# Kernel optimization log

Hardware: AMD Instinct MI355X
Metric: run time of the kernel (lower is better)

## Reference

```python
import jax, jax.numpy as jnp
import numpy as np

ALPHA = 0.1          # LeakyReLU negative slope
NEG = -9.0e15        # mask fill value (matches torch source)
S_OUT = 64           # source_out_features
T_OUT = 64           # target_out_features


def setup_inputs() -> dict:
    key = jax.random.key(0)
    ks = jax.random.split(key, 8)
    n_s, n_t = 8192, 4096
    s_in, t_in = 128, 128
    hs = jax.random.normal(ks[0], (n_s, s_in), dtype=jnp.float32)
    ht = jax.random.normal(ks[1], (n_t, t_in), dtype=jnp.float32)
    A_opt = jax.random.randint(ks[2], (n_t, n_s), 0, 2, dtype=jnp.int32)
    # xavier_uniform with gain=1.414
    def xavier(k, shape, gain=1.414):
        fan_in, fan_out = shape[0], shape[1]
        bound = gain * np.sqrt(6.0 / (fan_in + fan_out))
        return jax.random.uniform(k, shape, jnp.float32, -bound, bound)
    Ws = xavier(ks[3], (s_in, T_OUT))
    Wt = xavier(ks[4], (t_in, S_OUT))
    a1 = xavier(ks[5], (S_OUT + T_OUT, 1))
    bias_s = jnp.zeros((T_OUT,), jnp.float32)
    bias_t = jnp.zeros((S_OUT,), jnp.float32)
    return {"hs": hs, "ht": ht, "A_opt": A_opt, "Ws": Ws, "Wt": Wt,
            "a1": a1, "bias_s": bias_s, "bias_t": bias_t}


def reference(hs, ht, A_opt, Ws, Wt, a1, bias_s, bias_t):
    # Asymmetric HOAN, eval mode (dropout=0), concatenate=True.
    Whs = hs @ Ws                       # [n_s, t_out]
    Wht = ht @ Wt                       # [n_t, s_out]
    # a1 split: first S_OUT rows pair with Wht, remaining T_OUT rows with Whs
    a_t = a1[:S_OUT, :]                 # [s_out, 1]
    a_s = a1[S_OUT:, :]                 # [t_out, 1]
    Whst = Whs @ a_s                    # [n_s, 1]
    Whtt = Wht @ a_t                    # [n_t, 1]
    e_st = jax.nn.leaky_relu(Whtt + Whst.T, ALPHA)   # [n_t, n_s]
    e_ts = jax.nn.leaky_relu(Whst + Whtt.T, ALPHA)   # [n_s, n_t]
    mask = A_opt > 0                    # [n_t, n_s]
    att_st = jax.nn.softmax(jnp.where(mask, e_st, NEG), axis=1)
    h_prime_st = att_st @ Whs + bias_s  # [n_t, t_out]
    att_ts = jax.nn.softmax(jnp.where(mask.T, e_ts, NEG), axis=1)
    h_prime_ts = att_ts @ Wht + bias_t  # [n_s, s_out]
    return jax.nn.elu(h_prime_st), jax.nn.elu(h_prime_ts)
```

## Files before the change

### kernel.cpp

```cpp
#include <hip/hip_runtime.h>
#include <math.h>

#define N_S 8192
#define N_T 4096
#define DIN 128
#define NF  64
#define SPL0 8
#define SPL1 4

typedef __attribute__((ext_vector_type(8))) short short8;
typedef __attribute__((ext_vector_type(4))) float f32x4;
typedef __attribute__((ext_vector_type(4))) int i32x4;
typedef unsigned long long u64;
typedef unsigned int u32;

__device__ __forceinline__ unsigned short f2bf(float x){
  unsigned u = __float_as_uint(x);
  unsigned r = (u + 0x7fffu + ((u >> 16) & 1u)) >> 16;
  return (unsigned short)r;
}

__device__ __forceinline__ size_t xt2_idx(int f, int k){
  return ((size_t)(k >> 5))*2048 + (size_t)((f >> 4)*512 + ((k >> 3) & 3)*128 + (f & 15)*8 + (k & 7));
}

__global__ __launch_bounds__(256) void k1_fused(
    const int* __restrict__ A,
    u64* __restrict__ RBt,
    const float* __restrict__ hs, const float* __restrict__ ht,
    const float* __restrict__ Ws, const float* __restrict__ Wt,
    const float* __restrict__ a1,
    unsigned short* __restrict__ XT2s, unsigned short* __restrict__ XT2t,
    float* __restrict__ EFs, float* __restrict__ EFt)
{
  __shared__ __align__(16) float smem[DIN*NF + 4*DIN];
  int bx = blockIdx.x;
  int t = threadIdx.x;
  if (bx < 2048) {
    u64* rbS = (u64*)smem;
    int w = t >> 6, l = t & 63;
    int i = 2*bx + (w >> 1);
    int h = w & 1;
    const int* base = A + (size_t)i*N_S + h*4096;
    #pragma unroll
    for (int it = 0; it < 16; ++it) {
      i32x4 v = *(const i32x4*)(base + it*256 + 4*l);
      u32 nib = (v.x > 0 ? 1u : 0u) | (v.y > 0 ? 2u : 0u)
              | (v.z > 0 ? 4u : 0u) | (v.w > 0 ? 8u : 0u);
      u32 b8  = nib | (((u32)__shfl_xor((int)nib, 1, 64)) << 4);
      u32 b16 = b8  | (((u32)__shfl_xor((int)b8,  2, 64)) << 8);
      u32 b32 = b16 | (((u32)__shfl_xor((int)b16, 4, 64)) << 16);
      u32 hi  = (u32)__shfl_xor((int)b32, 8, 64);
      if ((l & 15) == 0)
        rbS[(size_t)(w>>1)*128 + h*64 + it*4 + (l>>4)] = (u64)b32 | ((u64)hi << 32);
    }
    __syncthreads();
    int wi = t >> 1, ri = t & 1;
    RBt[(size_t)wi*N_T + 2*bx + ri] = rbS[(size_t)ri*128 + wi];
  } else {
    int b = bx - 2048;
    float* Wl = smem;
    float* hrow = smem + DIN*NF;
    bool is_s = b < (N_S/4);
    const float* h; const float* W; const float* av;
    unsigned short* XT; float* EFd; int r0;
    if (is_s) { r0 = b*4;           h = hs; W = Ws; av = a1 + 64; XT = XT2s; EFd = EFs; }
    else      { r0 = (b - N_S/4)*4; h = ht; W = Wt; av = a1;      XT = XT2t; EFd = EFt; }
    for (int i = t; i < DIN*NF; i += 256) Wl[i] = W[i];
    for (int i = t; i < 4*DIN;  i += 256) hrow[i] = h[(size_t)r0*DIN + i];
    __syncthreads();
    int f = t & 63, sr = t >> 6;
    float acc = 0.f;
    #pragma unroll 8
    for (int k = 0; k < DIN; ++k) acc += hrow[sr*DIN + k] * Wl[k*NF + f];
    int r = r0 + sr;
    XT[xt2_idx(f, r)] = f2bf(acc);
    float p = acc * av[f];
    #pragma unroll
    for (int o = 32; o > 0; o >>= 1) p += __shfl_xor(p, o, 64);
    if (f == 0) { EFd[2*r] = __expf(p); EFd[2*r + 1] = __expf(0.1f*p); }
  }
}

__global__ __launch_bounds__(256) void btr_kernel(
    const u64* __restrict__ RBt,
    u64* __restrict__ CBt)
{
  int id = blockIdx.x*4 + (threadIdx.x >> 6);
  int l = threadIdx.x & 63;
  int jc = id >> 6, ic = id & 63;
  u64 x = RBt[(size_t)jc*N_T + ic*64 + l];
  const u64 MM[6] = {0x00000000FFFFFFFFull, 0x0000FFFF0000FFFFull, 0x00FF00FF00FF00FFull,
                     0x0F0F0F0F0F0F0F0Full, 0x3333333333333333ull, 0x5555555555555555ull};
  const int DD[6] = {32, 16, 8, 4, 2, 1};
  #pragma unroll
  for (int s = 0; s < 6; ++s) {
    int d = DD[s]; u64 M = MM[s];
    u32 ylo = (u32)__shfl_xor((int)(u32)x, d, 64);
    u32 yhi = (u32)__shfl_xor((int)(u32)(x >> 32), d, 64);
    u64 y = (u64)ylo | ((u64)yhi << 32);
    x = ((l & d) == 0) ? ((x & M) | ((y & M) << d))
                       : ((x & ~M) | ((y & ~M) >> d));
  }
  CBt[(size_t)ic*N_S + jc*64 + l] = x;
}

template<int DIR>
__device__ __forceinline__ void agg_body(
    int rb, int split,
    const u64* __restrict__ MBt,
    const float* __restrict__ EFu, const float* __restrict__ EFk,
    const unsigned short* __restrict__ XT2,
    float* __restrict__ accP,
    float* __restrict__ sumP)
{
  constexpr int NK = (DIR == 0) ? N_S : N_T;
  constexpr int NU = (DIR == 0) ? N_T : N_S;
  constexpr int SPL = (DIR == 0) ? SPL0 : SPL1;
  constexpr int KCH = NK / SPL;
  int t = threadIdx.x;
  int wave = t >> 6, l = t & 63;
  int row16 = l & 15, grp = l >> 4;
  int u = rb*64 + wave*16 + row16;
  float2 ef = *(const float2*)&EFu[2*u];
  float Eu = ef.x, Fu = ef.y;
  f32x4 acc[4];
  #pragma unroll
  for (int q = 0; q < 4; ++q) { acc[q][0]=0.f; acc[q][1]=0.f; acc[q][2]=0.f; acc[q][3]=0.f; }
  f32x4 accs; accs[0]=0.f; accs[1]=0.f; accs[2]=0.f; accs[3]=0.f;
  short8 bones;
  #pragma unroll
  for (int j = 0; j < 8; ++j) bones[j] = (short)0x3F80;
  int kc0 = split * KCH;

  #pragma unroll 2
  for (int k0 = kc0; k0 < kc0 + KCH; k0 += 64) {
    u64 mb = MBt[(size_t)(k0 >> 6)*NU + u];
    u32 mlo = (u32)mb, mhi = (u32)(mb >> 32);
    short8 af01[2];
    #pragma unroll
    for (int h = 0; h < 2; ++h) {
      int kb = k0 + 32*h + grp*8;
      float4 p0 = *(const float4*)&EFk[2*kb];
      float4 p1 = *(const float4*)&EFk[2*kb + 4];
      float4 p2 = *(const float4*)&EFk[2*kb + 8];
      float4 p3 = *(const float4*)&EFk[2*kb + 12];
      float wv[8];
      wv[0] = fmaxf(Eu*p0.x, Fu*p0.y); wv[1] = fmaxf(Eu*p0.z, Fu*p0.w);
      wv[2] = fmaxf(Eu*p1.x, Fu*p1.y); wv[3] = fmaxf(Eu*p1.z, Fu*p1.w);
      wv[4] = fmaxf(Eu*p2.x, Fu*p2.y); wv[5] = fmaxf(Eu*p2.z, Fu*p2.w);
      wv[6] = fmaxf(Eu*p3.x, Fu*p3.y); wv[7] = fmaxf(Eu*p3.z, Fu*p3.w);
      u32 bb = ((h ? mhi : mlo) >> (grp*8)) & 0xffu;
      union { u32 uu[4]; short8 v; } pk;
      #pragma unroll
      for (int p = 0; p < 4; ++p) {
        int j = 2*p;
        int slo = ((int)(bb << (31 - j))) >> 31;
        int shi = ((int)(bb << (30 - j))) >> 31;
        u32 msk = __builtin_amdgcn_perm((u32)shi, (u32)slo, 0x05040100u);
        u32 w01 = __builtin_amdgcn_perm(__float_as_uint(wv[j+1]),
                                        __float_as_uint(wv[j]), 0x07060302u);
        pk.uu[p] = w01 & msk;
      }
      af01[h] = pk.v;
    }
    const unsigned short* xb = XT2 + ((size_t)(k0 >> 5))*2048 + l*8;
    #pragma unroll
    for (int q = 0; q < 4; ++q) {
      short8 b0 = *(const short8*)(xb + q*512);
      short8 b1 = *(const short8*)(xb + 2048 + q*512);
      acc[q] = __builtin_amdgcn_mfma_f32_16x16x32_bf16(af01[0], b0, acc[q], 0, 0, 0);
      acc[q] = __builtin_amdgcn_mfma_f32_16x16x32_bf16(af01[1], b1, acc[q], 0, 0, 0);
    }
    accs = __builtin_amdgcn_mfma_f32_16x16x32_bf16(af01[0], bones, accs, 0, 0, 0);
    accs = __builtin_amdgcn_mfma_f32_16x16x32_bf16(af01[1], bones, accs, 0, 0, 0);
  }

  if (row16 == 0) {
    #pragma unroll
    for (int r = 0; r < 4; ++r)
      sumP[(size_t)split*NU + rb*64 + wave*16 + grp*4 + r] = accs[r];
  }
  float* ap = accP + (size_t)split*NU*NF;
  #pragma unroll
  for (int q = 0; q < 4; ++q) {
    #pragma unroll
    for (int r = 0; r < 4; ++r) {
      int uo = rb*64 + wave*16 + grp*4 + r;
      ap[(size_t)uo*NF + q*16 + row16] = acc[q][r];
    }
  }
}

__global__ __launch_bounds__(256, 8) void agg_fused(
    const u64* __restrict__ RBt, const u64* __restrict__ CBt,
    const float* __restrict__ EFs, const float* __restrict__ EFt,
    const unsigned short* __restrict__ XT2s, const unsigned short* __restrict__ XT2t,
    float* __restrict__ P0, float* __restrict__ S0,
    float* __restrict__ P1, float* __restrict__ S1)
{
  int b = blockIdx.x;
  if (b < 64*SPL0) {
    agg_body<0>(b & 63, b >> 6, RBt, EFt, EFs, XT2s, P0, S0);
  } else {
    int b2 = b - 64*SPL0;
    agg_body<1>(b2 & 127, b2 >> 7, CBt, EFs, EFt, XT2t, P1, S1);
  }
}

__global__ __launch_bounds__(256) void finalize_kernel(
    const float* __restrict__ P0, const float* __restrict__ S0,
    const float* __restrict__ P1, const float* __restrict__ S1,
    const float* __restrict__ bias_s, const float* __restrict__ bias_t,
    float* __restrict__ out)
{
  int tid = blockIdx.x*256 + threadIdx.x;
  const int n0 = N_T*NF/4;
  float4 a = make_float4(0.f, 0.f, 0.f, 0.f);
  float den = 0.f;
  float4 bias;
  if (tid < n0) {
    int u = tid >> 4, fq = (tid & 15)*4;
    #pragma unroll
    for (int s = 0; s < SPL0; ++s) {
      float4 p = *(const float4*)&P0[((size_t)s*N_T + u)*NF + fq];
      a.x += p.x; a.y += p.y; a.z += p.z; a.w += p.w;
      den += S0[(size_t)s*N_T + u];
    }
    bias = *(const float4*)&bias_s[fq];
  } else {
    int i2 = tid - n0;
    int u = i2 >> 4, fq = (i2 & 15)*4;
    #pragma unroll
    for (int s = 0; s < SPL1; ++s) {
      float4 p = *(const float4*)&P1[((size_t)s*N_S + u)*NF + fq];
      a.x += p.x; a.y += p.y; a.z += p.z; a.w += p.w;
      den += S1[(size_t)s*N_S + u];
    }
    bias = *(const float4*)&bias_t[fq];
  }
  float inv = den > 0.f ? 1.f/den : 0.f;
  float4 v;
  v.x = a.x*inv + bias.x; v.y = a.y*inv + bias.y;
  v.z = a.z*inv + bias.z; v.w = a.w*inv + bias.w;
  v.x = v.x > 0.f ? v.x : expm1f(v.x);
  v.y = v.y > 0.f ? v.y : expm1f(v.y);
  v.z = v.z > 0.f ? v.z : expm1f(v.z);
  v.w = v.w > 0.f ? v.w : expm1f(v.w);
  *(float4*)&out[tid*4] = v;
}

extern "C" void kernel_launch(void* const* d_in, const int* in_sizes, int n_in,
                              void* d_out, int out_size, void* d_ws, size_t ws_size,
                              hipStream_t stream)
{
  const float* hs     = (const float*)d_in[0];
  const float* ht     = (const float*)d_in[1];
  const int*   A      = (const int*)  d_in[2];
  const float* Ws     = (const float*)d_in[3];
  const float* Wt     = (const float*)d_in[4];
  const float* a1     = (const float*)d_in[5];
  const float* bias_s = (const float*)d_in[6];
  const float* bias_t = (const float*)d_in[7];
  float* out = (float*)d_out;

  u64* RBt = (u64*)d_ws;
  u64* CBt = RBt + (size_t)(N_S/64)*N_T;
  unsigned short* XT2s = (unsigned short*)(CBt + (size_t)(N_T/64)*N_S);
  unsigned short* XT2t = XT2s + (size_t)NF*N_S;
  float* EFs = (float*)(XT2t + (size_t)NF*N_T);
  float* EFt = EFs + 2*N_S;
  float* P0  = EFt + 2*N_T;
  float* S0  = P0 + (size_t)SPL0*N_T*NF;
  float* P1  = S0 + (size_t)SPL0*N_T;
  float* S1  = P1 + (size_t)SPL1*N_S*NF;

  k1_fused<<<2048 + (N_S + N_T)/4, 256, 0, stream>>>(A, RBt, hs, ht, Ws, Wt, a1,
                                                     XT2s, XT2t, EFs, EFt);
  btr_kernel<<<(N_S/64)*(N_T/64)/4, 256, 0, stream>>>(RBt, CBt);
  agg_fused<<<64*SPL0 + 128*SPL1, 256, 0, stream>>>(RBt, CBt, EFs, EFt, XT2s, XT2t,
                                                    P0, S0, P1, S1);
  finalize_kernel<<<(N_T*NF + N_S*NF)/1024, 256, 0, stream>>>(P0, S0, P1, S1,
                                                              bias_s, bias_t, out);
}
```

Before: 89.11 us.

## Fuse bitmask transpose into aggregation kernel via shared memory

Removes the separate bit-matrix transpose kernel and the transposed mask buffer. Direction-1 aggregation blocks now load their slice of the row mask, transpose the 64x64 bit tiles with wave shuffles, and stage them in shared memory before the main loop. This saves a kernel launch and a global write and read of the transposed mask. In exchange it adds per-block transpose work, 8KB of shared memory and a barrier, and the launch bound drops from 8 to 4 blocks per CU.

New measurement: 84.36 us. 1.06x faster.

```diff
diff --git a/kernel.cpp b/kernel.cpp
--- a/kernel.cpp
+++ b/kernel.cpp
@@ -82,37 +82,15 @@
   }
 }
 
-__global__ __launch_bounds__(256) void btr_kernel(
-    const u64* __restrict__ RBt,
-    u64* __restrict__ CBt)
-{
-  int id = blockIdx.x*4 + (threadIdx.x >> 6);
-  int l = threadIdx.x & 63;
-  int jc = id >> 6, ic = id & 63;
-  u64 x = RBt[(size_t)jc*N_T + ic*64 + l];
-  const u64 MM[6] = {0x00000000FFFFFFFFull, 0x0000FFFF0000FFFFull, 0x00FF00FF00FF00FFull,
-                     0x0F0F0F0F0F0F0F0Full, 0x3333333333333333ull, 0x5555555555555555ull};
-  const int DD[6] = {32, 16, 8, 4, 2, 1};
-  #pragma unroll
-  for (int s = 0; s < 6; ++s) {
-    int d = DD[s]; u64 M = MM[s];
-    u32 ylo = (u32)__shfl_xor((int)(u32)x, d, 64);
-    u32 yhi = (u32)__shfl_xor((int)(u32)(x >> 32), d, 64);
-    u64 y = (u64)ylo | ((u64)yhi << 32);
-    x = ((l & d) == 0) ? ((x & M) | ((y & M) << d))
-                       : ((x & ~M) | ((y & ~M) >> d));
-  }
-  CBt[(size_t)ic*N_S + jc*64 + l] = x;
-}
-
 template<int DIR>
 __device__ __forceinline__ void agg_body(
     int rb, int split,
-    const u64* __restrict__ MBt,
+    const u64* __restrict__ RBt,
     const float* __restrict__ EFu, const float* __restrict__ EFk,
     const unsigned short* __restrict__ XT2,
     float* __restrict__ accP,
-    float* __restrict__ sumP)
+    float* __restrict__ sumP,
+    u64* cbS)
 {
   constexpr int NK = (DIR == 0) ? N_S : N_T;
   constexpr int NU = (DIR == 0) ? N_T : N_S;
@@ -122,6 +100,30 @@
   int wave = t >> 6, l = t & 63;
   int row16 = l & 15, grp = l >> 4;
   int u = rb*64 + wave*16 + row16;
+  int kc0 = split * KCH;
+
+  if (DIR == 1) {
+    const u64 MM[6] = {0x00000000FFFFFFFFull, 0x0000FFFF0000FFFFull, 0x00FF00FF00FF00FFull,
+                       0x0F0F0F0F0F0F0F0Full, 0x3333333333333333ull, 0x5555555555555555ull};
+    const int DD[6] = {32, 16, 8, 4, 2, 1};
+    #pragma unroll
+    for (int cc = 0; cc < 4; ++cc) {
+      int c = wave*4 + cc;
+      u64 x = RBt[(size_t)rb*N_T + kc0 + c*64 + l];
+      #pragma unroll
+      for (int s = 0; s < 6; ++s) {
+        int d = DD[s]; u64 M = MM[s];
+        u32 ylo = (u32)__shfl_xor((int)(u32)x, d, 64);
+        u32 yhi = (u32)__shfl_xor((int)(u32)(x >> 32), d, 64);
+        u64 y = (u64)ylo | ((u64)yhi << 32);
+        x = ((l & d) == 0) ? ((x & M) | ((y & M) << d))
+                           : ((x & ~M) | ((y & ~M) >> d));
+      }
+      cbS[c*64 + l] = x;
+    }
+    __syncthreads();
+  }
+
   float2 ef = *(const float2*)&EFu[2*u];
   float Eu = ef.x, Fu = ef.y;
   f32x4 acc[4];
@@ -131,11 +133,11 @@
   short8 bones;
   #pragma unroll
   for (int j = 0; j < 8; ++j) bones[j] = (short)0x3F80;
-  int kc0 = split * KCH;
 
   #pragma unroll 2
   for (int k0 = kc0; k0 < kc0 + KCH; k0 += 64) {
-    u64 mb = MBt[(size_t)(k0 >> 6)*NU + u];
+    u64 mb = (DIR == 0) ? RBt[(size_t)(k0 >> 6)*NU + u]
+                        : cbS[((k0 - kc0) >> 6)*64 + wave*16 + row16];
     u32 mlo = (u32)mb, mhi = (u32)(mb >> 32);
     short8 af01[2];
     #pragma unroll
@@ -192,19 +194,20 @@
   }
 }
 
-__global__ __launch_bounds__(256, 8) void agg_fused(
-    const u64* __restrict__ RBt, const u64* __restrict__ CBt,
+__global__ __launch_bounds__(256, 4) void agg_fused(
+    const u64* __restrict__ RBt,
     const float* __restrict__ EFs, const float* __restrict__ EFt,
     const unsigned short* __restrict__ XT2s, const unsigned short* __restrict__ XT2t,
     float* __restrict__ P0, float* __restrict__ S0,
     float* __restrict__ P1, float* __restrict__ S1)
 {
+  __shared__ u64 cbS[16*64];
   int b = blockIdx.x;
   if (b < 64*SPL0) {
-    agg_body<0>(b & 63, b >> 6, RBt, EFt, EFs, XT2s, P0, S0);
+    agg_body<0>(b & 63, b >> 6, RBt, EFt, EFs, XT2s, P0, S0, cbS);
   } else {
     int b2 = b - 64*SPL0;
-    agg_body<1>(b2 & 127, b2 >> 7, CBt, EFs, EFt, XT2t, P1, S1);
+    agg_body<1>(b2 & 127, b2 >> 7, RBt, EFs, EFt, XT2t, P1, S1, cbS);
   }
 }
 
@@ -265,8 +268,7 @@
   float* out = (float*)d_out;
 
   u64* RBt = (u64*)d_ws;
-  u64* CBt = RBt + (size_t)(N_S/64)*N_T;
-  unsigned short* XT2s = (unsigned short*)(CBt + (size_t)(N_T/64)*N_S);
+  unsigned short* XT2s = (unsigned short*)(RBt + (size_t)(N_S/64)*N_T);
   unsigned short* XT2t = XT2s + (size_t)NF*N_S;
   float* EFs = (float*)(XT2t + (size_t)NF*N_T);
   float* EFt = EFs + 2*N_S;
@@ -277,8 +279,7 @@
 
   k1_fused<<<2048 + (N_S + N_T)/4, 256, 0, stream>>>(A, RBt, hs, ht, Ws, Wt, a1,
                                                      XT2s, XT2t, EFs, EFt);
-  btr_kernel<<<(N_S/64)*(N_T/64)/4, 256, 0, stream>>>(RBt, CBt);
-  agg_fused<<<64*SPL0 + 128*SPL1, 256, 0, stream>>>(RBt, CBt, EFs, EFt, XT2s, XT2t,
+  agg_fused<<<64*SPL0 + 128*SPL1, 256, 0, stream>>>(RBt, EFs, EFt, XT2s, XT2t,
                                                     P0, S0, P1, S1);
   finalize_kernel<<<(N_T*NF + N_S*NF)/1024, 256, 0, stream>>>(P0, S0, P1, S1,
                                                               bias_s, bias_t, out);
```
